# Optimization experiments

Measured on AMD Instinct MI355X. Metric: run time of the kernel, lower is better.

Reference implementation:

```python
import jax, jax.numpy as jnp
import numpy as np

B, D, M, H = 512, 2048, 32, 64  # batch, d_model, memory_length, memory_hidden_dims

def _glu(x):
    a, b = jnp.split(x, 2, axis=-1)
    return a * jax.nn.sigmoid(b)

def setup_inputs() -> dict:
    key = jax.random.key(0)
    k1, k2, k3 = jax.random.split(key, 3)
    s1 = 1.0 / np.sqrt(M + 2 * H)
    s2 = 1.0 / np.sqrt(H + 2)
    return {
        "state_trace": jax.random.normal(k1, (B, D, M), jnp.float32),
        "w1a": jax.random.uniform(k2, (M, 2 * H, D), jnp.float32, -s1, s1),
        "b1a": jnp.zeros((1, D, 2 * H), jnp.float32),
        "Ta": jnp.ones((1,), jnp.float32),
        "w1b": jax.random.uniform(k3, (H, 2, D), jnp.float32, -s2, s2),
        "b1b": jnp.zeros((1, D, 2), jnp.float32),
        "Tb": jnp.ones((1,), jnp.float32),
    }

def reference(state_trace, w1a, b1a, Ta, w1b, b1b, Tb):
    # SuperLinear 1: per-feature grouped matmul over d_model (D axis)
    x = (jnp.einsum('BDM,MHD->BDH', state_trace, w1a) + b1a) / Ta  # [B, D, 2H]
    x = _glu(x)                                                     # [B, D, H]
    # SuperLinear 2
    x = (jnp.einsum('BDM,MHD->BDH', x, w1b) + b1b) / Tb             # [B, D, 2]
    x = _glu(x)                                                     # [B, D, 1]
    return x.squeeze(-1)                                            # [B, D]
```

## Files before the change

### kernel.cpp

```cpp
#include <hip/hip_runtime.h>
#include <hip/hip_bf16.h>


#define NB 512
#define ND 2048
#define NM 32
#define NH 64

typedef __bf16 bf16x8 __attribute__((ext_vector_type(8)));
typedef float f32x4 __attribute__((ext_vector_type(4)));

#define LDS_STRIDE 40

__device__ __forceinline__ float sigmoid_fast(float x) {
    return __builtin_amdgcn_rcpf(1.0f + __builtin_amdgcn_exp2f(-1.442695040888963f * x));
}

__global__ __launch_bounds__(256) void nlm_fused(
    const float* __restrict__ st,
    const float* __restrict__ w1a,
    const float* __restrict__ b1a,
    const float* __restrict__ Ta,
    const float* __restrict__ w1b,
    const float* __restrict__ b1b,
    const float* __restrict__ Tb,
    float* __restrict__ out)
{
    __shared__ __bf16 w1_lds[128 * LDS_STRIDE];
    __shared__ float  w2_lds[128];

    const int bid  = blockIdx.x;
    const int d    = (bid & 7) * (ND / 8) + (bid >> 3);
    const int tid  = threadIdx.x;
    const int wave = tid >> 6;
    const int lane = tid & 63;
    const int l15  = lane & 15;
    const int lg   = lane >> 4;

    {
        const int h    = tid & 127;
        const int half = tid >> 7;
        #pragma unroll
        for (int i = 0; i < 16; ++i) {
            const int m = half * 16 + i;
            float v = w1a[(size_t)(m * 128 + h) * ND + d];
            w1_lds[h * LDS_STRIDE + m] = (__bf16)v;
        }
    }
    if (tid < 128) {
        w2_lds[tid] = w1b[(size_t)tid * ND + d];
    }

    const float rTa = 1.0f / Ta[0];
    const float rTb = 1.0f / Tb[0];
    const float bb0 = b1b[d * 2 + 0];
    const float bb1 = b1b[d * 2 + 1];

    f32x4 bias[8];
    #pragma unroll
    for (int t = 0; t < 8; ++t)
        bias[t] = *(const f32x4*)(b1a + (size_t)d * 128 + t * 16 + lg * 4);

    __syncthreads();

    bf16x8 afrag[8];
    #pragma unroll
    for (int t = 0; t < 8; ++t) {
        const int h = t * 16 + l15;
        afrag[t] = *(const bf16x8*)(&w1_lds[h * LDS_STRIDE + lg * 8]);
    }
    float w2a[4][4], w2b[4][4];
    #pragma unroll
    for (int t = 0; t < 4; ++t)
        #pragma unroll
        for (int r = 0; r < 4; ++r) {
            const int h = t * 16 + lg * 4 + r;
            w2a[t][r] = w2_lds[h * 2 + 0];
            w2b[t][r] = w2_lds[h * 2 + 1];
        }

    const int bbase = wave * 128;
    const float* sp0 = st + ((size_t)(bbase + l15) * ND + d) * NM + lg * 8;
    f32x4 s0 = *(const f32x4*)sp0;
    f32x4 s1 = *(const f32x4*)(sp0 + 4);

    for (int bt = 0; bt < 8; ++bt) {
        f32x4 c0 = s0, c1 = s1;
        if (bt < 7) {
            const float* sp = st + ((size_t)(bbase + (bt + 1) * 16 + l15) * ND + d) * NM + lg * 8;
            s0 = *(const f32x4*)sp;
            s1 = *(const f32x4*)(sp + 4);
        }
        bf16x8 bfrag;
        #pragma unroll
        for (int j = 0; j < 4; ++j) {
            bfrag[j]     = (__bf16)c0[j];
            bfrag[j + 4] = (__bf16)c1[j];
        }
        f32x4 acc[8];
        #pragma unroll
        for (int t = 0; t < 8; ++t) acc[t] = bias[t];
        #pragma unroll
        for (int t = 0; t < 8; ++t)
            acc[t] = __builtin_amdgcn_mfma_f32_16x16x32_bf16(afrag[t], bfrag, acc[t], 0, 0, 0);

        float z0 = 0.0f, z1 = 0.0f;
        #pragma unroll
        for (int t = 0; t < 4; ++t)
            #pragma unroll
            for (int r = 0; r < 4; ++r) {
                const float ya = acc[t][r]     * rTa;
                const float yb = acc[t + 4][r] * rTa;
                const float g  = ya * sigmoid_fast(yb);
                z0 = fmaf(g, w2a[t][r], z0);
                z1 = fmaf(g, w2b[t][r], z1);
            }
        z0 += __shfl_xor(z0, 16);
        z0 += __shfl_xor(z0, 32);
        z1 += __shfl_xor(z1, 16);
        z1 += __shfl_xor(z1, 32);
        if (lg == 0) {
            const float za = (z0 + bb0) * rTb;
            const float zb = (z1 + bb1) * rTb;
            out[(size_t)(bbase + bt * 16 + l15) * ND + d] = za * sigmoid_fast(zb);
        }
    }
}

extern "C" void kernel_launch(void* const* d_in, const int* in_sizes, int n_in,
                              void* d_out, int out_size, void* d_ws, size_t ws_size,
                              hipStream_t stream) {
    const float* st  = (const float*)d_in[0];
    const float* w1a = (const float*)d_in[1];
    const float* b1a = (const float*)d_in[2];
    const float* Ta  = (const float*)d_in[3];
    const float* w1b = (const float*)d_in[4];
    const float* b1b = (const float*)d_in[5];
    const float* Tb  = (const float*)d_in[6];
    float* out = (float*)d_out;

    nlm_fused<<<dim3(ND), dim3(256), 0, stream>>>(st, w1a, b1a, Ta, w1b, b1b, Tb, out);
}
```

Before: 261.2 us.

## Pre-transpose weights to per-feature bf16 layout in a separate kernel

Adds a transpose kernel that rewrites w1a into a per-d contiguous bf16 layout and w1b into a per-d contiguous layout in workspace. The main kernel then loads MFMA A-fragments and second-layer weights directly from global memory instead of doing strided scalar gathers into LDS. This removes uncoalesced stride-ND weight reads from the main kernel but adds a second launch and an extra pass over the weights every call.

```diff
diff --git a/kernel.cpp b/kernel.cpp
--- a/kernel.cpp
+++ b/kernel.cpp
@@ -5,79 +5,109 @@
 #define NB 512
 #define ND 2048
 #define NM 32
-#define NH 64
+#define NH2 128
 
 typedef __bf16 bf16x8 __attribute__((ext_vector_type(8)));
 typedef float f32x4 __attribute__((ext_vector_type(4)));
+typedef float f32x2 __attribute__((ext_vector_type(2)));
 
-#define LDS_STRIDE 40
+#define WSA_BYTES ((size_t)ND * NH2 * NM * 2)
 
 __device__ __forceinline__ float sigmoid_fast(float x) {
     return __builtin_amdgcn_rcpf(1.0f + __builtin_amdgcn_exp2f(-1.442695040888963f * x));
 }
 
+__global__ __launch_bounds__(256) void transpose_w(const float* __restrict__ w1a,
+                                                   const float* __restrict__ w1b,
+                                                   __bf16* __restrict__ wsA,
+                                                   float* __restrict__ wsB) {
+    __shared__ float tile[64 * 65];
+    const int tid = threadIdx.x;
+    if (blockIdx.x < 2048) {
+        const int h0 = (blockIdx.x & 63) * 2;
+        const int d0 = (blockIdx.x >> 6) * 64;
+        const int dc = tid & 63, wv = tid >> 6;
+        #pragma unroll
+        for (int k = 0; k < 16; ++k) {
+            const int rr = wv + 4 * k;
+            const int m = rr >> 1, hh = rr & 1;
+            tile[rr * 65 + dc] = w1a[(size_t)(m * 128 + h0 + hh) * ND + d0 + dc];
+        }
+        __syncthreads();
+        const int dloc = tid >> 2, seg = tid & 3;
+        bf16x8 u0, u1;
+        #pragma unroll
+        for (int i = 0; i < 8; ++i) {
+            const int q0 = seg * 16 + i;
+            u0[i] = (__bf16)tile[((q0 & 31) * 2 + (q0 >> 5)) * 65 + dloc];
+            const int q1 = seg * 16 + 8 + i;
+            u1[i] = (__bf16)tile[((q1 & 31) * 2 + (q1 >> 5)) * 65 + dloc];
+        }
+        __bf16* dst = wsA + (size_t)(d0 + dloc) * (NH2 * NM) + h0 * 32 + seg * 16;
+        *(bf16x8*)dst = u0;
+        *(bf16x8*)(dst + 8) = u1;
+    } else {
+        const int d0 = (blockIdx.x - 2048) * 16;
+        const int dcol = tid & 15, pr = tid >> 4;
+        #pragma unroll
+        for (int k = 0; k < 8; ++k) {
+            const int p = pr + 16 * k;
+            tile[p * 17 + dcol] = w1b[(size_t)p * ND + d0 + dcol];
+        }
+        __syncthreads();
+        const int dloc = tid >> 4, j = tid & 15;
+        #pragma unroll
+        for (int i = 0; i < 8; ++i) {
+            const int row = j * 8 + i;
+            wsB[(size_t)(d0 + dloc) * 128 + j * 8 + i] = tile[row * 17 + dloc];
+        }
+    }
+}
+
 __global__ __launch_bounds__(256) void nlm_fused(
-    const float* __restrict__ st,
-    const float* __restrict__ w1a,
-    const float* __restrict__ b1a,
-    const float* __restrict__ Ta,
-    const float* __restrict__ w1b,
-    const float* __restrict__ b1b,
-    const float* __restrict__ Tb,
-    float* __restrict__ out)
+    const float*  __restrict__ st,
+    const __bf16* __restrict__ wsA,
+    const float*  __restrict__ b1a,
+    const float*  __restrict__ Ta,
+    const float*  __restrict__ wsB,
+    const float*  __restrict__ b1b,
+    const float*  __restrict__ Tb,
+    float*        __restrict__ out)
 {
-    __shared__ __bf16 w1_lds[128 * LDS_STRIDE];
-    __shared__ float  w2_lds[128];
-
-    const int bid  = blockIdx.x;
-    const int d    = (bid & 7) * (ND / 8) + (bid >> 3);
+    const int d    = blockIdx.x;
     const int tid  = threadIdx.x;
     const int wave = tid >> 6;
     const int lane = tid & 63;
     const int l15  = lane & 15;
     const int lg   = lane >> 4;
 
-    {
-        const int h    = tid & 127;
-        const int half = tid >> 7;
-        #pragma unroll
-        for (int i = 0; i < 16; ++i) {
-            const int m = half * 16 + i;
-            float v = w1a[(size_t)(m * 128 + h) * ND + d];
-            w1_lds[h * LDS_STRIDE + m] = (__bf16)v;
-        }
-    }
-    if (tid < 128) {
-        w2_lds[tid] = w1b[(size_t)tid * ND + d];
-    }
-
-    const float rTa = 1.0f / Ta[0];
-    const float rTb = 1.0f / Tb[0];
-    const float bb0 = b1b[d * 2 + 0];
-    const float bb1 = b1b[d * 2 + 1];
+    const __bf16* wA = wsA + (size_t)d * (NH2 * NM);
+    bf16x8 afrag[8];
+    #pragma unroll
+    for (int t = 0; t < 8; ++t)
+        afrag[t] = *(const bf16x8*)(wA + (t * 16 + l15) * 32 + lg * 8);
 
     f32x4 bias[8];
     #pragma unroll
     for (int t = 0; t < 8; ++t)
         bias[t] = *(const f32x4*)(b1a + (size_t)d * 128 + t * 16 + lg * 4);
 
-    __syncthreads();
-
-    bf16x8 afrag[8];
-    #pragma unroll
-    for (int t = 0; t < 8; ++t) {
-        const int h = t * 16 + l15;
-        afrag[t] = *(const bf16x8*)(&w1_lds[h * LDS_STRIDE + lg * 8]);
-    }
+    const float* w2d = wsB + (size_t)d * 128;
     float w2a[4][4], w2b[4][4];
     #pragma unroll
     for (int t = 0; t < 4; ++t)
         #pragma unroll
         for (int r = 0; r < 4; ++r) {
             const int h = t * 16 + lg * 4 + r;
-            w2a[t][r] = w2_lds[h * 2 + 0];
-            w2b[t][r] = w2_lds[h * 2 + 1];
+            f32x2 p = *(const f32x2*)(w2d + h * 2);
+            w2a[t][r] = p[0];
+            w2b[t][r] = p[1];
         }
+
+    const float rTa = 1.0f / Ta[0];
+    const float rTb = 1.0f / Tb[0];
+    const float bb0 = b1b[d * 2 + 0];
+    const float bb1 = b1b[d * 2 + 1];
 
     const int bbase = wave * 128;
     const float* sp0 = st + ((size_t)(bbase + l15) * ND + d) * NM + lg * 8;
@@ -139,5 +169,9 @@
     const float* Tb  = (const float*)d_in[6];
     float* out = (float*)d_out;
 
-    nlm_fused<<<dim3(ND), dim3(256), 0, stream>>>(st, w1a, b1a, Ta, w1b, b1b, Tb, out);
+    __bf16* wsA = (__bf16*)d_ws;
+    float*  wsB = (float*)((char*)d_ws + WSA_BYTES);
+
+    transpose_w<<<dim3(2048 + 128), dim3(256), 0, stream>>>(w1a, w1b, wsA, wsB);
+    nlm_fused<<<dim3(ND), dim3(256), 0, stream>>>(st, wsA, b1a, Ta, wsB, b1b, Tb, out);
 }
```

After: 250.7 us. 4.0% less time.
